# Kernel tuning notes

Measured on AMD Instinct MI355X. Metric: run time of the kernel, lower is better.

The kernel has to match this reference:

```python
import jax, jax.numpy as jnp
import numpy as np
import itertools

K = 10            # GFM knn k
SHARP = 20.0      # GMCCE_Sharp
THRESH = 0.5      # GMCCE_Thres


def setup_inputs() -> dict:
    key = jax.random.key(0)
    ks = jax.random.split(key, 5)
    B, D, N = 4, 512, 2048
    return {
        "src_embedding": jax.random.normal(ks[0], (B, D, N), jnp.float32),
        "tgt_embedding": jax.random.normal(ks[1], (B, D, N), jnp.float32),
        "src": jax.random.normal(ks[2], (B, 3, N), jnp.float32),
        "tgt": jax.random.normal(ks[3], (B, 3, N), jnp.float32),
        "temperature": jax.random.uniform(ks[4], (B, 1), jnp.float32) + 0.5,
        "is_corr": 1,
    }


def _knn_tri(x, k, sigma=1.0):
    # x: [B,3,N] -> idx [B,N,k] of largest gaussian weights (nearest points)
    pts = x.transpose(0, 2, 1)                      # [B,N,3]
    sq = jnp.sum(pts * pts, -1)                     # [B,N]
    d2 = sq[:, :, None] + sq[:, None, :] - 2.0 * jnp.einsum('bnd,bmd->bnm', pts, pts)
    d2 = jnp.maximum(d2, 0.0)
    w = jnp.exp(-d2 / (2.0 * sigma ** 2))
    _, idx = jax.lax.top_k(w, k)
    return idx


def _get_tri(pcd, tri_idx):
    # pcd: [B,N,3], tri_idx: [B,N,P,3] point indices -> [B,N,P,3] sorted (0,0,area)
    B = pcd.shape[0]
    b = jnp.arange(B)[:, None, None, None]
    pts = pcd[b, tri_idx]                           # [B,N,P,3pts,3xyz]
    e1 = pts[..., 1, :] - pts[..., 0, :]
    e2 = pts[..., 2, :] - pts[..., 0, :]
    normals = jnp.cross(e1, e2)
    areas = 0.5 * jnp.linalg.norm(normals, axis=-1)  # [B,N,P]
    z = jnp.zeros_like(areas)
    return jnp.sort(jnp.stack([areas, z, z], -1), axis=-1)


def _gfm(src, tgt, Sharp, Threshold, k=10, eps=1e-6):
    # src: [B,3,N]; tgt: [B,N,3] (corr points)
    B, _, N = src.shape
    idx = _knn_tri(src, k)                                            # [B,N,k]
    pairs = np.asarray(list(itertools.combinations(range(k), 2)))     # [P,2], P=45
    idx_pairs = idx[:, :, pairs]                                      # [B,N,P,2]
    index = jnp.broadcast_to(jnp.arange(N)[None, :, None, None], (B, N, pairs.shape[0], 1))
    tri_idx = jnp.concatenate([index, idx_pairs], -1)                 # [B,N,P,3]
    ls = _get_tri(src.transpose(0, 2, 1), tri_idx)
    lt = _get_tri(tgt, tri_idx) + eps
    loss = jnp.sum((ls - lt) ** 2, -1) / jnp.sum((ls + lt) ** 2, -1)  # [B,N,P]
    loss = jnp.sort(loss, -1)
    reg = jnp.linalg.norm(ls - lt, axis=-1)                           # unsorted, as in torch
    loss = loss + 0.1 * reg
    med = jnp.median(loss, axis=-1, keepdims=True)
    loss = jnp.where(loss > 3.0 * med, 0.0, loss)
    loss = jnp.mean(jnp.sqrt(loss[:, :, :k] + eps), -1)               # [B,N]
    loss = loss - jnp.min(loss, -1, keepdims=True)
    w = 2.0 * jax.nn.sigmoid(-Sharp * loss)
    return jnp.where(w > Threshold, 1.0, 0.0)


def _procrustes(X, Y, w, eps=1e-7):
    # X,Y: [N,3]; w: [N]
    W1 = jnp.sum(jnp.abs(w))
    wn = jnp.broadcast_to(w[:, None], X.shape) / (W1 + eps)
    mux = jnp.sum(wn * X, 0, keepdims=True)
    muy = jnp.sum(wn * Y, 0, keepdims=True)
    Sxy = (Y - muy).T @ (wn * (X - mux))
    U, _, Vh = jnp.linalg.svd(Sxy)
    det = jnp.linalg.det(U) * jnp.linalg.det(Vh)
    d = jnp.where(det < 0.0, jnp.array([1.0, 1.0, -1.0]), jnp.array([1.0, 1.0, 1.0]))
    R = (U * d[None, :]) @ Vh
    t = muy[0] - R @ mux[0]
    return R, t


def reference(src_embedding, tgt_embedding, src, tgt, temperature, is_corr):
    B, _, N = src.shape
    d_k = src_embedding.shape[1]
    scores = jnp.einsum('bdn,bdm->bnm', src_embedding, tgt_embedding) / jnp.sqrt(jnp.float32(d_k))
    scores = jax.nn.softmax(10000.0 * scores, axis=-1)
    corres = jnp.argmax(scores, -1)                                   # [B,N]
    corr_tgt = jnp.einsum('bnm,bmd->bnd', scores, tgt.transpose(0, 2, 1))
    weight = _gfm(src, corr_tgt, SHARP, THRESH, K)                    # [B,N]
    src_t = src.transpose(0, 2, 1)
    tgt_t = tgt.transpose(0, 2, 1)
    src_corr = jnp.take_along_axis(tgt_t, corres[..., None], axis=1)  # [B,N,3]
    w_d = jax.lax.stop_gradient(weight)                               # torch detaches weight
    R, T = jax.vmap(_procrustes)(src_t, src_corr, w_d)
    return R, T, corres[..., None], weight[..., None]
```

## Files before the change

kernel.cpp:

```cpp
#include <hip/hip_runtime.h>
#include <math.h>

#define NPTS 2048
#define DIM  512
#define BATCH 4
#define KNN 10
#define NPAIR 45
#define MSPLIT 32
#define CSPLIT 8
#define CCHUNK (NPTS / CSPLIT)
#define KB (DIM / 16)

typedef _Float16 half8  __attribute__((ext_vector_type(8)));
typedef float    f32x16 __attribute__((ext_vector_type(16)));

__global__ __launch_bounds__(256) void transpose_split(
    const float* __restrict__ srcEmb, const float* __restrict__ tgtEmb,
    _Float16* __restrict__ srcT_hi, _Float16* __restrict__ srcT_lo,
    _Float16* __restrict__ tgtT_hi, _Float16* __restrict__ tgtT_lo)
{
    __shared__ float ldsT[32][65];
    int blk = blockIdx.x;
    const int nt    = blk & 31;
    const int dt    = (blk >> 5) & 15;
    const int b     = (blk >> 9) & 3;
    const int which = blk >> 11;
    const float* in = (which == 0 ? srcEmb : tgtEmb) + (size_t)b * DIM * NPTS;
    _Float16* outHi = (which == 0 ? srcT_hi : tgtT_hi) + (size_t)b * NPTS * DIM;
    _Float16* outLo = (which == 0 ? srcT_lo : tgtT_lo) + (size_t)b * NPTS * DIM;
    const int tid = threadIdx.x;
#pragma unroll
    for (int i = 0; i < 2; ++i) {
        int id = tid + i * 256;
        int r = id >> 4, c4 = id & 15;
        float4 v = *(const float4*)(in + (size_t)(dt * 32 + r) * NPTS + nt * 64 + c4 * 4);
        ldsT[r][c4 * 4 + 0] = v.x; ldsT[r][c4 * 4 + 1] = v.y;
        ldsT[r][c4 * 4 + 2] = v.z; ldsT[r][c4 * 4 + 3] = v.w;
    }
    __syncthreads();
    const int nrow = tid >> 2, dseg = (tid & 3) * 8;
    __align__(16) _Float16 hb[8];
    __align__(16) _Float16 lb[8];
#pragma unroll
    for (int j = 0; j < 8; ++j) {
        float a = ldsT[dseg + j][nrow];
        _Float16 h = (_Float16)a;
        float r = a - (float)h;
        hb[j] = h;
        lb[j] = (_Float16)(r * 2048.0f);
    }
    const int n  = nt * 64 + nrow;
    const int d0 = dt * 32 + dseg;
    size_t off = ((size_t)(n >> 5) * KB + (d0 >> 4)) * 512
               + (size_t)((d0 >> 3) & 1) * 256 + (size_t)(n & 31) * 8;
    *(half8*)(outHi + off) = *(half8*)hb;
    *(half8*)(outLo + off) = *(half8*)lb;
}

__global__ __launch_bounds__(256, 2) void gemm_argmax(
    const _Float16* __restrict__ Ahi, const _Float16* __restrict__ Alo,
    const _Float16* __restrict__ Bhi, const _Float16* __restrict__ Blo,
    float* __restrict__ partV, int* __restrict__ partI)
{
    __shared__ _Float16 smem[32 * 512];
    const int tid  = threadIdx.x;
    int blk = blockIdx.x;
    const int nt = blk & 15, mt = (blk >> 4) & 15, b = blk >> 8;
    const int lane = tid & 63, wave = tid >> 6;
    const int wm = (wave & 1) * 64, wn = (wave >> 1) * 64;

    const _Float16* baseArr =
        (wave == 0) ? Ahi : (wave == 1) ? Alo : (wave == 2) ? Bhi : Blo;
    const int rt = (wave < 2) ? mt : nt;
    const _Float16* gbase = baseArr + (size_t)b * NPTS * DIM
                          + (size_t)(rt * 4) * KB * 512 + (size_t)lane * 8;
    const int ldsW = wave * 8 * 512 + lane * 8;
    const int laneoff = lane * 8;

    f32x16 accH[2][2], accX[2][2];
#pragma unroll
    for (int mi = 0; mi < 2; ++mi)
#pragma unroll
        for (int ni = 0; ni < 2; ++ni)
#pragma unroll
            for (int r = 0; r < 16; ++r) { accH[mi][ni][r] = 0.f; accX[mi][ni][r] = 0.f; }

    half8 pf[8];
#pragma unroll
    for (int i = 0; i < 8; ++i)
        pf[i] = *(const half8*)(gbase + ((size_t)(i >> 1) * KB + (i & 1)) * 512);

    for (int t = 0; t < 16; ++t) {
#pragma unroll
        for (int i = 0; i < 8; ++i)
            *(half8*)&smem[ldsW + i * 512] = pf[i];
        __syncthreads();
        if (t < 15) {
#pragma unroll
            for (int i = 0; i < 8; ++i)
                pf[i] = *(const half8*)(gbase + ((size_t)(i >> 1) * KB + (2 * (t + 1) + (i & 1))) * 512);
        }
#pragma unroll
        for (int ks = 0; ks < 2; ++ks) {
            half8 aF[2][2], bF[2][2];
#pragma unroll
            for (int mi = 0; mi < 2; ++mi)
#pragma unroll
                for (int h = 0; h < 2; ++h)
                    aF[mi][h] = *(const half8*)&smem[(h * 8 + ((wave & 1) * 2 + mi) * 2 + ks) * 512 + laneoff];
#pragma unroll
            for (int ni = 0; ni < 2; ++ni)
#pragma unroll
                for (int h = 0; h < 2; ++h)
                    bF[ni][h] = *(const half8*)&smem[((2 + h) * 8 + ((wave >> 1) * 2 + ni) * 2 + ks) * 512 + laneoff];
#pragma unroll
            for (int mi = 0; mi < 2; ++mi)
#pragma unroll
                for (int ni = 0; ni < 2; ++ni) {
                    accH[mi][ni] = __builtin_amdgcn_mfma_f32_32x32x16_f16(aF[mi][0], bF[ni][0], accH[mi][ni], 0, 0, 0);
                    accX[mi][ni] = __builtin_amdgcn_mfma_f32_32x32x16_f16(aF[mi][0], bF[ni][1], accX[mi][ni], 0, 0, 0);
                    accX[mi][ni] = __builtin_amdgcn_mfma_f32_32x32x16_f16(aF[mi][1], bF[ni][0], accX[mi][ni], 0, 0, 0);
                }
        }
        __syncthreads();
    }

    const float inv2048 = 1.0f / 2048.0f;
#pragma unroll
    for (int ni = 0; ni < 2; ++ni) {
        float bv = -INFINITY; int bi = 0x7fffffff;
#pragma unroll
        for (int mi = 0; mi < 2; ++mi)
#pragma unroll
            for (int r = 0; r < 16; ++r) {
                float v = accH[mi][ni][r] + accX[mi][ni][r] * inv2048;
                int m = mt * 128 + wm + mi * 32 + (r & 3) + 8 * (r >> 2) + 4 * (lane >> 5);
                if (v > bv || (v == bv && m < bi)) { bv = v; bi = m; }
            }
        float ov = __shfl_xor(bv, 32);
        int   oi = __shfl_xor(bi, 32);
        if (ov > bv || (ov == bv && oi < bi)) { bv = ov; bi = oi; }
        if (lane < 32) {
            int n = nt * 128 + wn + ni * 32 + lane;
            int s = mt * 2 + (wm >> 6);
            partV[((size_t)b * NPTS + n) * MSPLIT + s] = bv;
            partI[((size_t)b * NPTS + n) * MSPLIT + s] = bi;
        }
    }
}

__global__ void argmax_combine(const float* __restrict__ partV,
                               const int* __restrict__ partI,
                               int* __restrict__ corres,
                               float* __restrict__ outCorres)
{
    const int g = blockIdx.x * 256 + threadIdx.x;
    if (g >= BATCH * NPTS) return;
    float bv = -INFINITY; int bi = 0x7fffffff;
    for (int s = 0; s < MSPLIT; ++s) {
        float v = partV[(size_t)g * MSPLIT + s];
        int  ii = partI[(size_t)g * MSPLIT + s];
        if (v > bv || (v == bv && ii < bi)) { bv = v; bi = ii; }
    }
    corres[g] = bi;
    outCorres[g] = (float)bi;
}

__global__ __launch_bounds__(256, 8) void knn_part(
    const float* __restrict__ src,
    unsigned int* __restrict__ partK, int* __restrict__ partI)
{
    __shared__ float4 cpts[CCHUNK];
    __shared__ unsigned int   candK[CSPLIT][32][KNN];
    __shared__ unsigned short candI[CSPLIT][32][KNN];

    int blk = blockIdx.x;
    const int cs = blk & 7;  blk >>= 3;
    const int qg = blk & 63; blk >>= 6;
    const int b  = blk;
    const int tid = threadIdx.x;
    const float* S = src + (size_t)b * 3 * NPTS;

    {
        const int m = cs * CCHUNK + tid;
        float qx = S[m], qy = S[NPTS + m], qz = S[2 * NPTS + m];
        float qq = __fadd_rn(__fadd_rn(__fmul_rn(qx, qx), __fmul_rn(qy, qy)), __fmul_rn(qz, qz));
        cpts[tid] = make_float4(qx, qy, qz, qq);
    }
    __syncthreads();

    const int nl = tid & 31;
    const int sl = tid >> 5;
    const int n  = qg * 32 + nl;
    const float px = S[n], py = S[NPTS + n], pz = S[2 * NPTS + n];
    const float psq = __fadd_rn(__fadd_rn(__fmul_rn(px, px), __fmul_rn(py, py)), __fmul_rn(pz, pz));

    unsigned int bk[KNN]; int bi[KNN];
#pragma unroll
    for (int j = 0; j < KNN; ++j) { bk[j] = 0u; bi[j] = 0; }

    const int t0 = sl * 32;
    for (int j = 0; j < 32; ++j) {
        const int t = t0 + j;
        float4 c = cpts[t];
        float dot = __fadd_rn(__fadd_rn(__fmul_rn(px, c.x), __fmul_rn(py, c.y)), __fmul_rn(pz, c.z));
        float d2  = __fsub_rn(__fadd_rn(psq, c.w), __fmul_rn(2.f, dot));
        d2 = fmaxf(d2, 0.f);
        float w = expf(-0.5f * d2);
        unsigned int k = __float_as_uint(w);
        if (k > bk[KNN - 1]) {
            unsigned int ck = k; int ci = cs * CCHUNK + t;
#pragma unroll
            for (int q = 0; q < KNN; ++q) {
                bool gt = ck > bk[q];
                unsigned int tk = bk[q]; int ti = bi[q];
                bk[q] = gt ? ck : tk;  bi[q] = gt ? ci : ti;
                ck    = gt ? tk : ck;  ci    = gt ? ti : ci;
            }
        }
    }
#pragma unroll
    for (int j = 0; j < KNN; ++j) {
        candK[sl][nl][j] = bk[j];
        candI[sl][nl][j] = (unsigned short)bi[j];
    }
    __syncthreads();

    if (tid < 32) {
        int cur[CSPLIT] = {0, 0, 0, 0, 0, 0, 0, 0};
        const size_t base = (((size_t)b * NPTS + qg * 32 + tid) * CSPLIT + cs) * KNN;
        for (int sel = 0; sel < KNN; ++sel) {
            unsigned int bw = 0u; int bi2 = 0x7fffffff; int bs = -1;
#pragma unroll
            for (int s = 0; s < CSPLIT; ++s) {
                if (cur[s] < KNN) {
                    unsigned int k2 = candK[s][tid][cur[s]];
                    int i2 = (int)candI[s][tid][cur[s]];
                    if (k2 > bw || (k2 == bw && i2 < bi2)) { bw = k2; bi2 = i2; bs = s; }
                }
            }
            partK[base + sel] = bw;
            partI[base + sel] = bi2;
#pragma unroll
            for (int s = 0; s < CSPLIT; ++s) if (s == bs) cur[s]++;
        }
    }
}

__global__ void knn_merge(const unsigned int* __restrict__ partK,
                          const int* __restrict__ partI,
                          int* __restrict__ knnIdx)
{
    const int g = blockIdx.x * 256 + threadIdx.x;
    if (g >= BATCH * NPTS) return;
    const size_t base = (size_t)g * CSPLIT * KNN;
    int cur[CSPLIT] = {0, 0, 0, 0, 0, 0, 0, 0};
    for (int sel = 0; sel < KNN; ++sel) {
        unsigned int bw = 0u; int bi = 0x7fffffff; int bs = -1;
#pragma unroll
        for (int s = 0; s < CSPLIT; ++s) {
            if (cur[s] < KNN) {
                unsigned int k2 = partK[base + s * KNN + cur[s]];
                int i2 = partI[base + s * KNN + cur[s]];
                if (k2 > bw || (k2 == bw && i2 < bi)) { bw = k2; bi = i2; bs = s; }
            }
        }
        knnIdx[(size_t)g * KNN + sel] = bi;
#pragma unroll
        for (int s = 0; s < CSPLIT; ++s) if (s == bs) cur[s]++;
    }
}

__device__ const int PAIR_A[NPAIR] = {
    0,0,0,0,0,0,0,0,0, 1,1,1,1,1,1,1,1, 2,2,2,2,2,2,2,
    3,3,3,3,3,3, 4,4,4,4,4, 5,5,5,5, 6,6,6, 7,7, 8};
__device__ const int PAIR_C[NPAIR] = {
    1,2,3,4,5,6,7,8,9, 2,3,4,5,6,7,8,9, 3,4,5,6,7,8,9,
    4,5,6,7,8,9, 5,6,7,8,9, 6,7,8,9, 7,8,9, 8,9, 9};

__global__ __launch_bounds__(256) void loss_kernel(
    const float* __restrict__ src, const float* __restrict__ tgt,
    const int* __restrict__ corres, const int* __restrict__ knn,
    float* __restrict__ lossOut)
{
    const int wave = threadIdx.x >> 6;
    const int lane = threadIdx.x & 63;
    const int g = blockIdx.x * 4 + wave;
    const int b = g >> 11;
    const int n = g & (NPTS - 1);
    const float* S = src + (size_t)b * 3 * NPTS;
    const float* T = tgt + (size_t)b * 3 * NPTS;
    const int* cor = corres + b * NPTS;

    const float eps = 1e-6f;
    const float e2 = __fmul_rn(eps, eps);
    const float two_e2 = __fadd_rn(e2, e2);

    float Lv = INFINITY, Rv = 0.f;
    if (lane < NPAIR) {
        const int a = PAIR_A[lane], c = PAIR_C[lane];
        const int ia = knn[(size_t)g * KNN + a];
        const int ic = knn[(size_t)g * KNN + c];
        const float P0x = S[n], P0y = S[NPTS + n], P0z = S[2 * NPTS + n];
        const int c0 = cor[n];
        const float Q0x = T[c0], Q0y = T[NPTS + c0], Q0z = T[2 * NPTS + c0];

        float e1x = S[ia] - P0x, e1y = S[NPTS + ia] - P0y, e1z = S[2 * NPTS + ia] - P0z;
        float g2x = S[ic] - P0x, g2y = S[NPTS + ic] - P0y, g2z = S[2 * NPTS + ic] - P0z;
        float nx = __fsub_rn(__fmul_rn(e1y, g2z), __fmul_rn(e1z, g2y));
        float ny = __fsub_rn(__fmul_rn(e1z, g2x), __fmul_rn(e1x, g2z));
        float nz = __fsub_rn(__fmul_rn(e1x, g2y), __fmul_rn(e1y, g2x));
        float as_ = 0.5f * sqrtf(__fadd_rn(__fadd_rn(__fmul_rn(nx, nx), __fmul_rn(ny, ny)), __fmul_rn(nz, nz)));

        const int ca = cor[ia], cc = cor[ic];
        float f1x = T[ca] - Q0x, f1y = T[NPTS + ca] - Q0y, f1z = T[2 * NPTS + ca] - Q0z;
        float h2x = T[cc] - Q0x, h2y = T[NPTS + cc] - Q0y, h2z = T[2 * NPTS + cc] - Q0z;
        float mx = __fsub_rn(__fmul_rn(f1y, h2z), __fmul_rn(f1z, h2y));
        float my = __fsub_rn(__fmul_rn(f1z, h2x), __fmul_rn(f1x, h2z));
        float mz = __fsub_rn(__fmul_rn(f1x, h2y), __fmul_rn(f1y, h2x));
        float at_ = 0.5f * sqrtf(__fadd_rn(__fadd_rn(__fmul_rn(mx, mx), __fmul_rn(my, my)), __fmul_rn(mz, mz)));

        float lt3 = __fadd_rn(at_, eps);
        float d  = __fsub_rn(as_, lt3);
        float s  = __fadd_rn(as_, lt3);
        float num = __fadd_rn(two_e2, __fmul_rn(d, d));
        float den = __fadd_rn(two_e2, __fmul_rn(s, s));
        Lv = num / den;
        Rv = sqrtf(num);
    }

    float sl = Lv;
#pragma unroll
    for (int k = 2; k <= 64; k <<= 1)
#pragma unroll
        for (int j = k >> 1; j > 0; j >>= 1) {
            float other = __shfl_xor(sl, j);
            bool up = ((lane & k) == 0);
            bool lower = ((lane & j) == 0);
            sl = (up == lower) ? fminf(sl, other) : fmaxf(sl, other);
        }

    float comb = __fadd_rn(sl, __fmul_rn(0.1f, Rv));
    if (lane >= NPAIR) comb = INFINITY;

    float cs = comb;
#pragma unroll
    for (int k = 2; k <= 64; k <<= 1)
#pragma unroll
        for (int j = k >> 1; j > 0; j >>= 1) {
            float other = __shfl_xor(cs, j);
            bool up = ((lane & k) == 0);
            bool lower = ((lane & j) == 0);
            cs = (up == lower) ? fminf(cs, other) : fmaxf(cs, other);
        }
    float med = __shfl(cs, 22);
    float thr = __fmul_rn(3.0f, med);

    float v = 0.f;
    if (lane < KNN) {
        float x = comb;
        if (x > thr) x = 0.f;
        v = sqrtf(__fadd_rn(x, eps));
    }
#pragma unroll
    for (int j = 32; j > 0; j >>= 1) v += __shfl_xor(v, j);
    if (lane == 0) lossOut[g] = v / 10.0f;
}

__global__ void min_kernel(const float* __restrict__ loss, float* __restrict__ minOut)
{
    __shared__ float red[256];
    const int b = blockIdx.x;
    float m = INFINITY;
    for (int n = threadIdx.x; n < NPTS; n += 256) m = fminf(m, loss[b * NPTS + n]);
    red[threadIdx.x] = m; __syncthreads();
    for (int s = 128; s > 0; s >>= 1) {
        if (threadIdx.x < s) red[threadIdx.x] = fminf(red[threadIdx.x], red[threadIdx.x + s]);
        __syncthreads();
    }
    if (threadIdx.x == 0) minOut[b] = red[0];
}

__global__ void weight_kernel(const float* __restrict__ loss, const float* __restrict__ minv,
                              float* __restrict__ wOut, float* __restrict__ wWs)
{
    const int g = blockIdx.x * 256 + threadIdx.x;
    if (g >= BATCH * NPTS) return;
    const int b = g >> 11;
    float l = __fsub_rn(loss[g], minv[b]);
    float el = expf(20.0f * l);
    float sg = 1.0f / (1.0f + el);
    float w = 2.0f * sg;
    float res = (w > 0.5f) ? 1.0f : 0.0f;
    wOut[g] = res;
    wWs[g] = res;
}

__device__ inline double det3(const double M[3][3])
{
    return M[0][0] * (M[1][1] * M[2][2] - M[1][2] * M[2][1])
         - M[0][1] * (M[1][0] * M[2][2] - M[1][2] * M[2][0])
         + M[0][2] * (M[1][0] * M[2][1] - M[1][1] * M[2][0]);
}

__global__ __launch_bounds__(256) void procrustes_kernel(
    const float* __restrict__ src, const float* __restrict__ tgt,
    const int* __restrict__ corres, const float* __restrict__ weight,
    float* __restrict__ outRT)
{
    __shared__ double red[256];
    __shared__ double sh[16];
    const int b = blockIdx.x;
    const int tid = threadIdx.x;
    const float* S = src + (size_t)b * 3 * NPTS;
    const float* T = tgt + (size_t)b * 3 * NPTS;
    const int* cor = corres + b * NPTS;
    const float* w = weight + b * NPTS;

    double a7[7] = {0, 0, 0, 0, 0, 0, 0};
    for (int n = tid; n < NPTS; n += 256) {
        double wn = w[n];
        if (wn != 0.0) {
            double x0 = S[n], x1 = S[NPTS + n], x2 = S[2 * NPTS + n];
            int c = cor[n];
            double y0 = T[c], y1 = T[NPTS + c], y2 = T[2 * NPTS + c];
            a7[0] += wn;
            a7[1] += wn * x0; a7[2] += wn * x1; a7[3] += wn * x2;
            a7[4] += wn * y0; a7[5] += wn * y1; a7[6] += wn * y2;
        }
    }
    for (int q = 0; q < 7; ++q) {
        red[tid] = a7[q]; __syncthreads();
        for (int s2 = 128; s2 > 0; s2 >>= 1) {
            if (tid < s2) red[tid] += red[tid + s2];
            __syncthreads();
        }
        if (tid == 0) sh[q] = red[0];
        __syncthreads();
    }
    const double W1 = sh[0];
    const double denom = W1 + 1e-7;
    const double mux0 = sh[1] / denom, mux1 = sh[2] / denom, mux2 = sh[3] / denom;
    const double muy0 = sh[4] / denom, muy1 = sh[5] / denom, muy2 = sh[6] / denom;

    double a9[9] = {0, 0, 0, 0, 0, 0, 0, 0, 0};
    for (int n = tid; n < NPTS; n += 256) {
        double wn = w[n];
        if (wn != 0.0) {
            double ww = wn / denom;
            double x0 = ww * ((double)S[n] - mux0);
            double x1 = ww * ((double)S[NPTS + n] - mux1);
            double x2 = ww * ((double)S[2 * NPTS + n] - mux2);
            int c = cor[n];
            double y0 = (double)T[c] - muy0;
            double y1 = (double)T[NPTS + c] - muy1;
            double y2 = (double)T[2 * NPTS + c] - muy2;
            a9[0] += y0 * x0; a9[1] += y0 * x1; a9[2] += y0 * x2;
            a9[3] += y1 * x0; a9[4] += y1 * x1; a9[5] += y1 * x2;
            a9[6] += y2 * x0; a9[7] += y2 * x1; a9[8] += y2 * x2;
        }
    }
    for (int q = 0; q < 9; ++q) {
        red[tid] = a9[q]; __syncthreads();
        for (int s2 = 128; s2 > 0; s2 >>= 1) {
            if (tid < s2) red[tid] += red[tid + s2];
            __syncthreads();
        }
        if (tid == 0) sh[q] = red[0];
        __syncthreads();
    }

    if (tid == 0) {
        double Ae[3][3] = {{sh[0], sh[1], sh[2]}, {sh[3], sh[4], sh[5]}, {sh[6], sh[7], sh[8]}};
        double M[3][3], V[3][3] = {{1, 0, 0}, {0, 1, 0}, {0, 0, 1}};
        for (int i = 0; i < 3; ++i)
            for (int j = 0; j < 3; ++j) {
                double s2 = 0;
                for (int k = 0; k < 3; ++k) s2 += Ae[k][i] * Ae[k][j];
                M[i][j] = s2;
            }
        const int pp[3] = {0, 0, 1}, qq[3] = {1, 2, 2};
        for (int sweep = 0; sweep < 60; ++sweep) {
            double off = fabs(M[0][1]) + fabs(M[0][2]) + fabs(M[1][2]);
            if (off < 1e-30) break;
            for (int e = 0; e < 3; ++e) {
                int p = pp[e], q = qq[e];
                double apq = M[p][q];
                if (fabs(apq) < 1e-300) continue;
                double app = M[p][p], aqq = M[q][q];
                double theta = (aqq - app) / (2.0 * apq);
                double t = ((theta >= 0) ? 1.0 : -1.0) / (fabs(theta) + sqrt(theta * theta + 1.0));
                double cc = 1.0 / sqrt(t * t + 1.0), ss = t * cc;
                int r = 3 - p - q;
                double mrp = M[r][p], mrq = M[r][q];
                M[p][p] = app - t * apq;
                M[q][q] = aqq + t * apq;
                M[p][q] = M[q][p] = 0.0;
                M[r][p] = M[p][r] = cc * mrp - ss * mrq;
                M[r][q] = M[q][r] = ss * mrp + cc * mrq;
                for (int k = 0; k < 3; ++k) {
                    double vp = V[k][p], vq = V[k][q];
                    V[k][p] = cc * vp - ss * vq;
                    V[k][q] = ss * vp + cc * vq;
                }
            }
        }
        double ev[3] = {M[0][0], M[1][1], M[2][2]};
        int o[3] = {0, 1, 2};
        for (int i = 0; i < 2; ++i)
            for (int j = 0; j < 2 - i; ++j)
                if (ev[o[j]] < ev[o[j + 1]]) { int tswap = o[j]; o[j] = o[j + 1]; o[j + 1] = tswap; }
        double Vs[3][3], Us[3][3], sig[3];
        for (int k = 0; k < 3; ++k) {
            sig[k] = sqrt(fmax(ev[o[k]], 0.0));
            for (int i = 0; i < 3; ++i) Vs[i][k] = V[i][o[k]];
        }
        for (int k = 0; k < 3; ++k) {
            double u0 = Ae[0][0] * Vs[0][k] + Ae[0][1] * Vs[1][k] + Ae[0][2] * Vs[2][k];
            double u1 = Ae[1][0] * Vs[0][k] + Ae[1][1] * Vs[1][k] + Ae[1][2] * Vs[2][k];
            double u2 = Ae[2][0] * Vs[0][k] + Ae[2][1] * Vs[1][k] + Ae[2][2] * Vs[2][k];
            if (sig[k] > 1e-12 * sig[0] + 1e-300) {
                Us[0][k] = u0 / sig[k]; Us[1][k] = u1 / sig[k]; Us[2][k] = u2 / sig[k];
            } else if (k == 2) {
                double cx = Us[1][0] * Us[2][1] - Us[2][0] * Us[1][1];
                double cy = Us[2][0] * Us[0][1] - Us[0][0] * Us[2][1];
                double cz = Us[0][0] * Us[1][1] - Us[1][0] * Us[0][1];
                double nn = sqrt(cx * cx + cy * cy + cz * cz);
                if (nn < 1e-300) { cx = 0; cy = 0; cz = 1; nn = 1; }
                Us[0][2] = cx / nn; Us[1][2] = cy / nn; Us[2][2] = cz / nn;
            } else {
                Us[0][k] = (k == 0) ? 1 : 0; Us[1][k] = (k == 1) ? 1 : 0; Us[2][k] = 0;
            }
        }
        double detU = det3(Us), detV = det3(Vs);
        double dsg = (detU * detV < 0.0) ? -1.0 : 1.0;
        double R[3][3];
        for (int i = 0; i < 3; ++i)
            for (int j = 0; j < 3; ++j) {
                R[i][j] = Us[i][0] * Vs[j][0] + Us[i][1] * Vs[j][1] + dsg * Us[i][2] * Vs[j][2];
                outRT[b * 9 + i * 3 + j] = (float)R[i][j];
            }
        double mu_x[3] = {mux0, mux1, mux2};
        double mu_y[3] = {muy0, muy1, muy2};
        for (int i = 0; i < 3; ++i) {
            double ti = mu_y[i] - (R[i][0] * mu_x[0] + R[i][1] * mu_x[1] + R[i][2] * mu_x[2]);
            outRT[36 + b * 3 + i] = (float)ti;
        }
    }
}

extern "C" void kernel_launch(void* const* d_in, const int* in_sizes, int n_in,
                              void* d_out, int out_size, void* d_ws, size_t ws_size,
                              hipStream_t stream)
{
    const float* srcEmb = (const float*)d_in[0];
    const float* tgtEmb = (const float*)d_in[1];
    const float* src    = (const float*)d_in[2];
    const float* tgt    = (const float*)d_in[3];
    float* out = (float*)d_out;

    char* wsp = (char*)d_ws;
    const size_t TSZ = (size_t)BATCH * NPTS * DIM * sizeof(_Float16);
    _Float16* tgtT_hi = (_Float16*)wsp;                 wsp += TSZ;
    _Float16* tgtT_lo = (_Float16*)wsp;                 wsp += TSZ;
    _Float16* srcT_hi = (_Float16*)wsp;                 wsp += TSZ;
    _Float16* srcT_lo = (_Float16*)wsp;                 wsp += TSZ;
    float* wsPartV = (float*)wsp;                       wsp += (size_t)BATCH * NPTS * MSPLIT * 4;
    int*   wsPartI = (int*)wsp;                         wsp += (size_t)BATCH * NPTS * MSPLIT * 4;
    int*   wsCorres = (int*)wsp;                        wsp += BATCH * NPTS * 4;
    int*   wsKnn    = (int*)wsp;                        wsp += BATCH * NPTS * KNN * 4;
    float* wsLoss   = (float*)wsp;                      wsp += BATCH * NPTS * 4;
    float* wsMin    = (float*)wsp;                      wsp += 256;
    float* wsWeight = (float*)wsp;                      wsp += BATCH * NPTS * 4;

    unsigned int* knnPartK = (unsigned int*)tgtT_hi;
    int*          knnPartI = (int*)tgtT_lo;

    float* outCorres = out + 48;
    float* outWeight = out + 48 + BATCH * NPTS;

    transpose_split<<<dim3(4096), dim3(256), 0, stream>>>(
        srcEmb, tgtEmb, srcT_hi, srcT_lo, tgtT_hi, tgtT_lo);
    gemm_argmax<<<dim3(1024), dim3(256), 0, stream>>>(
        tgtT_hi, tgtT_lo, srcT_hi, srcT_lo, wsPartV, wsPartI);
    argmax_combine<<<dim3((BATCH * NPTS + 255) / 256), dim3(256), 0, stream>>>(
        wsPartV, wsPartI, wsCorres, outCorres);
    knn_part<<<dim3(BATCH * 64 * CSPLIT), dim3(256), 0, stream>>>(src, knnPartK, knnPartI);
    knn_merge<<<dim3((BATCH * NPTS + 255) / 256), dim3(256), 0, stream>>>(
        knnPartK, knnPartI, wsKnn);
    loss_kernel<<<dim3(BATCH * NPTS / 4), dim3(256), 0, stream>>>(
        src, tgt, wsCorres, wsKnn, wsLoss);
    min_kernel<<<dim3(BATCH), dim3(256), 0, stream>>>(wsLoss, wsMin);
    weight_kernel<<<dim3((BATCH * NPTS + 255) / 256), dim3(256), 0, stream>>>(
        wsLoss, wsMin, outWeight, wsWeight);
    procrustes_kernel<<<dim3(BATCH), dim3(256), 0, stream>>>(
        src, tgt, wsCorres, wsWeight, out);
}
```

Measured before the change: 184.1 us.

## Load MFMA fragments directly from global with register double-buffering, swizzle blocks

The GEMM-argmax kernel drops its LDS staging and both barriers per K step. Each wave now loads its own A/B hi/lo fragments straight from global memory into two register sets that alternate between load and MFMA. Block indices are remapped so that neighbouring blocks run on different XCDs and groups share tiles in cache. The KNN partial buffers move into dedicated workspace instead of aliasing the transposed tensors, which adds workspace use; each wave now reads duplicated data from global/L2 without shared reuse.

```diff
diff --git a/kernel.cpp b/kernel.cpp
--- a/kernel.cpp
+++ b/kernel.cpp
@@ -62,20 +62,28 @@
     const _Float16* __restrict__ Bhi, const _Float16* __restrict__ Blo,
     float* __restrict__ partV, int* __restrict__ partI)
 {
-    __shared__ _Float16 smem[32 * 512];
-    const int tid  = threadIdx.x;
-    int blk = blockIdx.x;
+    const int tid = threadIdx.x;
+    const int p = blockIdx.x;
+    const int blk = (p & 7) * 128 + (p >> 3);
     const int nt = blk & 15, mt = (blk >> 4) & 15, b = blk >> 8;
     const int lane = tid & 63, wave = tid >> 6;
     const int wm = (wave & 1) * 64, wn = (wave >> 1) * 64;
 
-    const _Float16* baseArr =
-        (wave == 0) ? Ahi : (wave == 1) ? Alo : (wave == 2) ? Bhi : Blo;
-    const int rt = (wave < 2) ? mt : nt;
-    const _Float16* gbase = baseArr + (size_t)b * NPTS * DIM
-                          + (size_t)(rt * 4) * KB * 512 + (size_t)lane * 8;
-    const int ldsW = wave * 8 * 512 + lane * 8;
-    const int laneoff = lane * 8;
+    const size_t bbase = (size_t)b * NPTS * DIM + (size_t)lane * 8;
+    const _Float16* aH[2]; const _Float16* aL[2];
+    const _Float16* bH[2]; const _Float16* bL[2];
+#pragma unroll
+    for (int mi = 0; mi < 2; ++mi) {
+        size_t rb = (size_t)(mt * 4 + (wm >> 5) + mi) * KB * 512;
+        aH[mi] = Ahi + bbase + rb;
+        aL[mi] = Alo + bbase + rb;
+    }
+#pragma unroll
+    for (int ni = 0; ni < 2; ++ni) {
+        size_t rb = (size_t)(nt * 4 + (wn >> 5) + ni) * KB * 512;
+        bH[ni] = Bhi + bbase + rb;
+        bL[ni] = Blo + bbase + rb;
+    }
 
     f32x16 accH[2][2], accX[2][2];
 #pragma unroll
@@ -85,45 +93,42 @@
 #pragma unroll
             for (int r = 0; r < 16; ++r) { accH[mi][ni][r] = 0.f; accX[mi][ni][r] = 0.f; }
 
-    half8 pf[8];
-#pragma unroll
-    for (int i = 0; i < 8; ++i)
-        pf[i] = *(const half8*)(gbase + ((size_t)(i >> 1) * KB + (i & 1)) * 512);
-
-    for (int t = 0; t < 16; ++t) {
-#pragma unroll
-        for (int i = 0; i < 8; ++i)
-            *(half8*)&smem[ldsW + i * 512] = pf[i];
-        __syncthreads();
-        if (t < 15) {
-#pragma unroll
-            for (int i = 0; i < 8; ++i)
-                pf[i] = *(const half8*)(gbase + ((size_t)(i >> 1) * KB + (2 * (t + 1) + (i & 1))) * 512);
-        }
-#pragma unroll
-        for (int ks = 0; ks < 2; ++ks) {
-            half8 aF[2][2], bF[2][2];
-#pragma unroll
-            for (int mi = 0; mi < 2; ++mi)
-#pragma unroll
-                for (int h = 0; h < 2; ++h)
-                    aF[mi][h] = *(const half8*)&smem[(h * 8 + ((wave & 1) * 2 + mi) * 2 + ks) * 512 + laneoff];
-#pragma unroll
-            for (int ni = 0; ni < 2; ++ni)
-#pragma unroll
-                for (int h = 0; h < 2; ++h)
-                    bF[ni][h] = *(const half8*)&smem[((2 + h) * 8 + ((wave >> 1) * 2 + ni) * 2 + ks) * 512 + laneoff];
-#pragma unroll
-            for (int mi = 0; mi < 2; ++mi)
-#pragma unroll
-                for (int ni = 0; ni < 2; ++ni) {
-                    accH[mi][ni] = __builtin_amdgcn_mfma_f32_32x32x16_f16(aF[mi][0], bF[ni][0], accH[mi][ni], 0, 0, 0);
-                    accX[mi][ni] = __builtin_amdgcn_mfma_f32_32x32x16_f16(aF[mi][0], bF[ni][1], accX[mi][ni], 0, 0, 0);
-                    accX[mi][ni] = __builtin_amdgcn_mfma_f32_32x32x16_f16(aF[mi][1], bF[ni][0], accX[mi][ni], 0, 0, 0);
-                }
-        }
-        __syncthreads();
-    }
+#define LOADSET(SA, SLA, SB, SLB, kb)                                        \
+    {                                                                        \
+        _Pragma("unroll")                                                    \
+        for (int q = 0; q < 2; ++q) {                                        \
+            SA[q]  = *(const half8*)(aH[q] + (size_t)(kb) * 512);            \
+            SLA[q] = *(const half8*)(aL[q] + (size_t)(kb) * 512);            \
+            SB[q]  = *(const half8*)(bH[q] + (size_t)(kb) * 512);            \
+            SLB[q] = *(const half8*)(bL[q] + (size_t)(kb) * 512);            \
+        }                                                                    \
+    }
+#define MFMASET(SA, SLA, SB, SLB)                                            \
+    {                                                                        \
+        _Pragma("unroll")                                                    \
+        for (int mi = 0; mi < 2; ++mi)                                       \
+            _Pragma("unroll")                                                \
+            for (int ni = 0; ni < 2; ++ni) {                                 \
+                accH[mi][ni] = __builtin_amdgcn_mfma_f32_32x32x16_f16(       \
+                    SA[mi], SB[ni], accH[mi][ni], 0, 0, 0);                  \
+                accX[mi][ni] = __builtin_amdgcn_mfma_f32_32x32x16_f16(       \
+                    SA[mi], SLB[ni], accX[mi][ni], 0, 0, 0);                 \
+                accX[mi][ni] = __builtin_amdgcn_mfma_f32_32x32x16_f16(       \
+                    SLA[mi], SB[ni], accX[mi][ni], 0, 0, 0);                 \
+            }                                                                \
+    }
+
+    half8 eA[2], eLa[2], eB[2], eLb[2];
+    half8 oA[2], oLa[2], oB[2], oLb[2];
+    LOADSET(eA, eLa, eB, eLb, 0)
+    for (int kb = 0; kb < KB; kb += 2) {
+        LOADSET(oA, oLa, oB, oLb, kb + 1)
+        MFMASET(eA, eLa, eB, eLb)
+        if (kb + 2 < KB) LOADSET(eA, eLa, eB, eLb, kb + 2)
+        MFMASET(oA, oLa, oB, oLb)
+    }
+#undef LOADSET
+#undef MFMASET
 
     const float inv2048 = 1.0f / 2048.0f;
 #pragma unroll
@@ -565,16 +570,15 @@
     _Float16* tgtT_lo = (_Float16*)wsp;                 wsp += TSZ;
     _Float16* srcT_hi = (_Float16*)wsp;                 wsp += TSZ;
     _Float16* srcT_lo = (_Float16*)wsp;                 wsp += TSZ;
-    float* wsPartV = (float*)wsp;                       wsp += (size_t)BATCH * NPTS * MSPLIT * 4;
-    int*   wsPartI = (int*)wsp;                         wsp += (size_t)BATCH * NPTS * MSPLIT * 4;
+    float* wsPartV  = (float*)wsp;                      wsp += (size_t)BATCH * NPTS * MSPLIT * 4;
+    int*   wsPartI  = (int*)wsp;                        wsp += (size_t)BATCH * NPTS * MSPLIT * 4;
     int*   wsCorres = (int*)wsp;                        wsp += BATCH * NPTS * 4;
     int*   wsKnn    = (int*)wsp;                        wsp += BATCH * NPTS * KNN * 4;
     float* wsLoss   = (float*)wsp;                      wsp += BATCH * NPTS * 4;
     float* wsMin    = (float*)wsp;                      wsp += 256;
     float* wsWeight = (float*)wsp;                      wsp += BATCH * NPTS * 4;
-
-    unsigned int* knnPartK = (unsigned int*)tgtT_hi;
-    int*          knnPartI = (int*)tgtT_lo;
+    unsigned int* knnPartK = (unsigned int*)wsp;        wsp += (size_t)BATCH * NPTS * CSPLIT * KNN * 4;
+    int*          knnPartI = (int*)wsp;                 wsp += (size_t)BATCH * NPTS * CSPLIT * KNN * 4;
 
     float* outCorres = out + 48;
     float* outWeight = out + 48 + BATCH * NPTS;
```

Result: no change. 184.9 us (+0.4%).
